# Kernel tuning notes

Hardware: AMD Instinct MI355X
Metric: run time of the kernel (lower is better)

## Reference

```python
import jax, jax.numpy as jnp
from jax import lax
import numpy as np

REG = 0.1  # regularization_strength
EPS = 1e-12  # F.normalize clamp


def pav_nonincreasing(y):
    """Pool-Adjacent-Violators: argmin_v ||v - y||^2 s.t. v_1 >= v_2 >= ... >= v_n.
    Stack-based O(n) sweep, jit-compatible (fixed shapes)."""
    n = y.shape[0]
    sums0 = jnp.zeros(n, y.dtype)
    cnts0 = jnp.zeros(n, y.dtype)

    def body(i, state):
        sums, cnts, ptr = state
        cur_s = y[i]
        cur_c = jnp.asarray(1.0, y.dtype)

        def cond(c):
            cs, cc, p, sm, ct = c
            j = jnp.maximum(p - 1, 0)
            # merge while prev block mean < current mean (violates nonincreasing)
            return (p > 0) & (sm[j] * cc < cs * ct[j])

        def merge(c):
            cs, cc, p, sm, ct = c
            return (cs + sm[p - 1], cc + ct[p - 1], p - 1, sm, ct)

        cs, cc, p, sums, cnts = lax.while_loop(cond, merge, (cur_s, cur_c, ptr, sums, cnts))
        sums = sums.at[p].set(cs)
        cnts = cnts.at[p].set(cc)
        return (sums, cnts, p + 1)

    sums, cnts, ptr = lax.fori_loop(0, n, body, (sums0, cnts0, jnp.int32(0)))
    means = sums / jnp.maximum(cnts, 1)
    bounds = jnp.cumsum(cnts)  # block end positions; bounds[ptr-1] == n, stale tail harmless
    bid = jnp.searchsorted(bounds, jnp.arange(n, dtype=y.dtype) + 0.5)
    return means[bid]


def soft_rank_desc_row(values):
    """fast-soft-sort soft_rank, direction='DESCENDING', regularization='l2'.
    Projection of values*scale onto permutahedron(n..1) via isotonic regression."""
    n = values.shape[0]
    scale = -1.0 / REG  # DESCENDING => sign = -1
    z = values * scale
    perm = jnp.argsort(-z)           # sort z descending
    s = z[perm]
    w = jnp.arange(n, 0, -1, dtype=values.dtype)  # n, n-1, ..., 1
    dual = pav_nonincreasing(s - w)
    primal = s - dual
    inv = jnp.argsort(perm)
    return primal[inv]


def setup_inputs() -> dict:
    key = jax.random.key(0)
    kq, kc = jax.random.split(key)
    query_embed = jax.random.normal(kq, (16, 384), dtype=jnp.float32)
    corpus_embeds = jax.random.normal(kc, (50000, 384), dtype=jnp.float32)
    return {"query_embed": query_embed, "corpus_embeds": corpus_embeds, "k": 100}


def reference(query_embed, corpus_embeds, k):
    q = query_embed / jnp.maximum(
        jnp.linalg.norm(query_embed, axis=-1, keepdims=True), EPS)
    c = corpus_embeds / jnp.maximum(
        jnp.linalg.norm(corpus_embeds, axis=-1, keepdims=True), EPS)
    similarities = q @ c.T  # (batch, num_docs) cosine sims
    soft_ranks = jax.vmap(soft_rank_desc_row)(similarities)
    return similarities, soft_ranks
```

## Files before the change

### kernel.cpp

```cpp
#include <hip/hip_runtime.h>
#include <hip/hip_bf16.h>

#define NQ 16
#define DIM 384
#define NBINS 64

typedef __attribute__((ext_vector_type(8))) short bf16x8;
typedef __attribute__((ext_vector_type(4))) float f32x4;

__global__ __launch_bounds__(128) void norm_q_kernel(
    const float* __restrict__ q, __hip_bfloat16* __restrict__ qbf,
    float* __restrict__ sums) {
  int b = blockIdx.x, t = threadIdx.x;
  float ss = 0.f;
  for (int k = t; k < DIM; k += 128) {
    float x = q[b * DIM + k];
    ss += x * x;
  }
  #pragma unroll
  for (int o = 32; o > 0; o >>= 1) ss += __shfl_down(ss, o, 64);
  __shared__ float wsum[2];
  if ((t & 63) == 0) wsum[t >> 6] = ss;
  __syncthreads();
  float inv = 1.0f / fmaxf(sqrtf(wsum[0] + wsum[1]), 1e-12f);
  for (int k = t; k < DIM; k += 128)
    qbf[b * DIM + k] = __float2bfloat16(q[b * DIM + k] * inv);
  if (t < NBINS) sums[b * NBINS + t] = 0.f;
}

__global__ __launch_bounds__(256, 6) void sim_mfma_kernel(
    const float* __restrict__ corpus, const __hip_bfloat16* __restrict__ qbf,
    float* __restrict__ out_sims, float* __restrict__ sums, int n) {
  int lane = threadIdx.x & 63;
  int w = threadIdx.x >> 6;
  int col = lane & 15;
  int quad = lane >> 4;
  int doc = blockIdx.x * 16 + col;
  int dload = doc < n ? doc : n - 1;

  const float* crow = corpus + (size_t)dload * DIM + quad * 8;
  const __hip_bfloat16* qrow = qbf + col * DIM + quad * 8;

  float4 v[6];
  #pragma unroll
  for (int s = 0; s < 3; ++s) {
    int ks = w + 4 * s;
    v[2 * s] = *reinterpret_cast<const float4*>(crow + ks * 32);
    v[2 * s + 1] = *reinterpret_cast<const float4*>(crow + ks * 32 + 4);
  }

  f32x4 acc = {0.f, 0.f, 0.f, 0.f};
  float nrm2 = 0.f;
  #pragma unroll
  for (int s = 0; s < 3; ++s) {
    int ks = w + 4 * s;
    bf16x8 a = *reinterpret_cast<const bf16x8*>(qrow + ks * 32);
    float4 v0 = v[2 * s], v1 = v[2 * s + 1];
    nrm2 += v0.x * v0.x + v0.y * v0.y + v0.z * v0.z + v0.w * v0.w +
            v1.x * v1.x + v1.y * v1.y + v1.z * v1.z + v1.w * v1.w;
    union { bf16x8 b; __hip_bfloat162 h[4]; } u;
    u.h[0] = __float22bfloat162_rn(float2{v0.x, v0.y});
    u.h[1] = __float22bfloat162_rn(float2{v0.z, v0.w});
    u.h[2] = __float22bfloat162_rn(float2{v1.x, v1.y});
    u.h[3] = __float22bfloat162_rn(float2{v1.z, v1.w});
    acc = __builtin_amdgcn_mfma_f32_16x16x32_bf16(a, u.b, acc, 0, 0, 0);
  }

  __shared__ float part[4][64 * 5];
  float* myp = &part[w][lane * 5];
  myp[0] = acc[0]; myp[1] = acc[1]; myp[2] = acc[2]; myp[3] = acc[3];
  myp[4] = nrm2;
  __syncthreads();

  if (w == 0) {
    float a0 = 0.f, a1 = 0.f, a2 = 0.f, a3 = 0.f, nn = 0.f;
    #pragma unroll
    for (int ww = 0; ww < 4; ++ww) {
      const float* p = &part[ww][lane * 5];
      a0 += p[0]; a1 += p[1]; a2 += p[2]; a3 += p[3]; nn += p[4];
    }
    nn += __shfl_xor(nn, 16, 64);
    nn += __shfl_xor(nn, 32, 64);
    float inv = 1.0f / fmaxf(sqrtf(nn), 1e-12f);

    bool valid = doc < n;
    float s4[4] = {a0 * inv, a1 * inv, a2 * inv, a3 * inv};
    int bin = blockIdx.x & (NBINS - 1);
    #pragma unroll
    for (int i = 0; i < 4; ++i) {
      if (valid) out_sims[(size_t)(quad * 4 + i) * n + doc] = s4[i];
      float vr = valid ? s4[i] : 0.f;
      #pragma unroll
      for (int o = 1; o < 16; o <<= 1) vr += __shfl_xor(vr, o, 64);
      if (col == 0) atomicAdd(&sums[(quad * 4 + i) * NBINS + bin], vr);
    }
  }
}

__global__ __launch_bounds__(256) void rank4_kernel(
    const float4* __restrict__ sims4, const float* __restrict__ sums,
    float4* __restrict__ out4, int n4, float half_np1, float inv_n) {
  int b = blockIdx.y;
  float bsum = sums[b * NBINS + (threadIdx.x & 63)];
  #pragma unroll
  for (int o = 32; o > 0; o >>= 1) bsum += __shfl_xor(bsum, o, 64);
  int i = blockIdx.x * 256 + threadIdx.x;
  if (i >= n4) return;
  float base = 10.0f * bsum * inv_n + half_np1;
  float4 v = sims4[(size_t)b * n4 + i];
  float4 r;
  r.x = base - 10.0f * v.x;
  r.y = base - 10.0f * v.y;
  r.z = base - 10.0f * v.z;
  r.w = base - 10.0f * v.w;
  out4[(size_t)b * n4 + i] = r;
}

__global__ __launch_bounds__(256) void rank1_kernel(
    const float* __restrict__ sims, const float* __restrict__ sums,
    float* __restrict__ out, int n, float half_np1, float inv_n) {
  int b = blockIdx.y;
  float bsum = sums[b * NBINS + (threadIdx.x & 63)];
  #pragma unroll
  for (int o = 32; o > 0; o >>= 1) bsum += __shfl_xor(bsum, o, 64);
  int i = blockIdx.x * 256 + threadIdx.x;
  if (i >= n) return;
  float base = 10.0f * bsum * inv_n + half_np1;
  out[(size_t)b * n + i] = base - 10.0f * sims[(size_t)b * n + i];
}

extern "C" void kernel_launch(void* const* d_in, const int* in_sizes, int n_in,
                              void* d_out, int out_size, void* d_ws,
                              size_t ws_size, hipStream_t stream) {
  const float* q = (const float*)d_in[0];
  const float* corpus = (const float*)d_in[1];
  int n = in_sizes[1] / DIM;
  float* out = (float*)d_out;
  float* ranks = out + (size_t)NQ * n;

  float* ws_f = (float*)d_ws;
  float* sums = ws_f;
  __hip_bfloat16* qbf = (__hip_bfloat16*)(ws_f + NQ * NBINS);

  norm_q_kernel<<<NQ, 128, 0, stream>>>(q, qbf, sums);
  sim_mfma_kernel<<<(n + 15) / 16, 256, 0, stream>>>(corpus, qbf, out, sums, n);

  float half_np1 = 0.5f * (float)(n + 1);
  float inv_n = 1.0f / (float)n;
  if ((n & 3) == 0) {
    int n4 = n >> 2;
    dim3 g((n4 + 255) / 256, NQ);
    rank4_kernel<<<g, 256, 0, stream>>>((const float4*)out, sums,
                                        (float4*)ranks, n4, half_np1, inv_n);
  } else {
    dim3 g((n + 255) / 256, NQ);
    rank1_kernel<<<g, 256, 0, stream>>>(out, sums, ranks, n, half_np1, inv_n);
  }
}
```

Baseline: 125.0 us.

## Stage corpus tile through LDS with fully coalesced loads and bf16 packing

The corpus rows for each 16-document block are now loaded cooperatively by all 256 threads as contiguous float4 reads. They are converted to bf16 and written into a padded shared-memory stage, then read back as MFMA B fragments. Before, each lane read strided 32-byte chunks straight from global memory. The norm is now computed from the bf16-rounded values, which changes precision slightly, and the change adds an LDS round trip, a barrier and extra shared memory per block. Occupancy is also raised from 6 to 7 in the launch bounds.

Measured after the change: 123.9 us. Within noise of the previous version (-0.9%).

```diff
diff --git a/kernel.cpp b/kernel.cpp
--- a/kernel.cpp
+++ b/kernel.cpp
@@ -4,9 +4,18 @@
 #define NQ 16
 #define DIM 384
 #define NBINS 64
+#define DPB 16
+#define ROWB 784
 
 typedef __attribute__((ext_vector_type(8))) short bf16x8;
 typedef __attribute__((ext_vector_type(4))) float f32x4;
+
+static __device__ inline unsigned pack_bf16x2(float a, float b) {
+  __hip_bfloat162 h = __float22bfloat162_rn(float2{a, b});
+  union { __hip_bfloat162 h; unsigned u; } c;
+  c.h = h;
+  return c.u;
+}
 
 __global__ __launch_bounds__(128) void norm_q_kernel(
     const float* __restrict__ q, __hip_bfloat16* __restrict__ qbf,
@@ -28,51 +37,73 @@
   if (t < NBINS) sums[b * NBINS + t] = 0.f;
 }
 
-__global__ __launch_bounds__(256, 6) void sim_mfma_kernel(
+__global__ __launch_bounds__(256, 7) void sim_mfma_kernel(
     const float* __restrict__ corpus, const __hip_bfloat16* __restrict__ qbf,
     float* __restrict__ out_sims, float* __restrict__ sums, int n) {
-  int lane = threadIdx.x & 63;
-  int w = threadIdx.x >> 6;
+  __shared__ __align__(16) unsigned char stage[DPB * ROWB];
+  __shared__ float part[4][64 * 5];
+
+  int tid = threadIdx.x;
+  int lane = tid & 63;
+  int w = tid >> 6;
   int col = lane & 15;
   int quad = lane >> 4;
-  int doc = blockIdx.x * 16 + col;
-  int dload = doc < n ? doc : n - 1;
 
-  const float* crow = corpus + (size_t)dload * DIM + quad * 8;
-  const __hip_bfloat16* qrow = qbf + col * DIM + quad * 8;
+  bf16x8 afrag[3];
+  {
+    const __hip_bfloat16* qrow = qbf + col * DIM + quad * 8;
+    #pragma unroll
+    for (int s = 0; s < 3; ++s)
+      afrag[s] = *reinterpret_cast<const bf16x8*>(qrow + (w + 4 * s) * 32);
+  }
 
-  float4 v[6];
-  #pragma unroll
-  for (int s = 0; s < 3; ++s) {
-    int ks = w + 4 * s;
-    v[2 * s] = *reinterpret_cast<const float4*>(crow + ks * 32);
-    v[2 * s + 1] = *reinterpret_cast<const float4*>(crow + ks * 32 + 4);
+  {
+    float4 v[6];
+    const float4* base = reinterpret_cast<const float4*>(corpus);
+    #pragma unroll
+    for (int it = 0; it < 6; ++it) {
+      int g = it * 256 + tid;
+      int row = g / 96;
+      int rem = g - row * 96;
+      int grow = blockIdx.x * DPB + row;
+      if (grow >= n) grow = n - 1;
+      v[it] = base[(size_t)grow * 96 + rem];
+    }
+    #pragma unroll
+    for (int it = 0; it < 6; ++it) {
+      int g = it * 256 + tid;
+      int row = g / 96;
+      int rem = g - row * 96;
+      uint2 pk;
+      pk.x = pack_bf16x2(v[it].x, v[it].y);
+      pk.y = pack_bf16x2(v[it].z, v[it].w);
+      *reinterpret_cast<uint2*>(&stage[row * ROWB + rem * 8]) = pk;
+    }
   }
+  __syncthreads();
 
   f32x4 acc = {0.f, 0.f, 0.f, 0.f};
   float nrm2 = 0.f;
   #pragma unroll
   for (int s = 0; s < 3; ++s) {
     int ks = w + 4 * s;
-    bf16x8 a = *reinterpret_cast<const bf16x8*>(qrow + ks * 32);
-    float4 v0 = v[2 * s], v1 = v[2 * s + 1];
-    nrm2 += v0.x * v0.x + v0.y * v0.y + v0.z * v0.z + v0.w * v0.w +
-            v1.x * v1.x + v1.y * v1.y + v1.z * v1.z + v1.w * v1.w;
-    union { bf16x8 b; __hip_bfloat162 h[4]; } u;
-    u.h[0] = __float22bfloat162_rn(float2{v0.x, v0.y});
-    u.h[1] = __float22bfloat162_rn(float2{v0.z, v0.w});
-    u.h[2] = __float22bfloat162_rn(float2{v1.x, v1.y});
-    u.h[3] = __float22bfloat162_rn(float2{v1.z, v1.w});
-    acc = __builtin_amdgcn_mfma_f32_16x16x32_bf16(a, u.b, acc, 0, 0, 0);
+    bf16x8 b = *reinterpret_cast<const bf16x8*>(
+        &stage[col * ROWB + ks * 64 + quad * 16]);
+    #pragma unroll
+    for (int j = 0; j < 8; ++j) {
+      float x = __uint_as_float(((unsigned)(unsigned short)b[j]) << 16);
+      nrm2 += x * x;
+    }
+    acc = __builtin_amdgcn_mfma_f32_16x16x32_bf16(afrag[s], b, acc, 0, 0, 0);
   }
 
-  __shared__ float part[4][64 * 5];
   float* myp = &part[w][lane * 5];
   myp[0] = acc[0]; myp[1] = acc[1]; myp[2] = acc[2]; myp[3] = acc[3];
   myp[4] = nrm2;
   __syncthreads();
 
   if (w == 0) {
+    int doc = blockIdx.x * DPB + col;
     float a0 = 0.f, a1 = 0.f, a2 = 0.f, a3 = 0.f, nn = 0.f;
     #pragma unroll
     for (int ww = 0; ww < 4; ++ww) {
@@ -143,7 +174,8 @@
   __hip_bfloat16* qbf = (__hip_bfloat16*)(ws_f + NQ * NBINS);
 
   norm_q_kernel<<<NQ, 128, 0, stream>>>(q, qbf, sums);
-  sim_mfma_kernel<<<(n + 15) / 16, 256, 0, stream>>>(corpus, qbf, out, sums, n);
+  sim_mfma_kernel<<<(n + DPB - 1) / DPB, 256, 0, stream>>>(corpus, qbf, out,
+                                                           sums, n);
 
   float half_np1 = 0.5f * (float)(n + 1);
   float inv_n = 1.0f / (float)n;
```
